# Optimization experiments

Hardware: AMD Instinct MI355X
Metric: run time of the kernel (lower is better)

## Reference

```python
import jax, jax.numpy as jnp
import numpy as np
from jax import lax

L = 4          # num_layers
DIM = 1024
HEADS = 4
DH = DIM // HEADS
MLP_H = 4 * DIM
EPS = 1e-5
SCALE = 1.0 / (DIM ** 0.5)  # note: module scales by 1/sqrt(dim), not 1/sqrt(head_dim)


def layer_norm(x, g, b):
    mu = jnp.mean(x, axis=-1, keepdims=True)
    var = jnp.var(x, axis=-1, keepdims=True)
    return (x - mu) * jax.lax.rsqrt(var + EPS) * g + b


def setup_inputs() -> dict:
    key = jax.random.key(0)
    ks = jax.random.split(key, 12)
    s = 0.02
    img = jax.random.normal(ks[0], (2, 2, 16, 192, 192), dtype=jnp.float32)
    conv_w = jax.random.normal(ks[1], (DIM, 2, 2, 8, 8), dtype=jnp.float32) * s
    conv_b = jnp.zeros((DIM,), jnp.float32)
    n_tokens = 24 * 24 * 8
    pos = jax.random.normal(ks[2], (1, n_tokens, DIM), dtype=jnp.float32) * s
    ln1_g = jnp.ones((L, DIM), jnp.float32); ln1_b = jnp.zeros((L, DIM), jnp.float32)
    ln2_g = jnp.ones((L, DIM), jnp.float32); ln2_b = jnp.zeros((L, DIM), jnp.float32)
    qkv_w = jax.random.normal(ks[3], (L, DIM, 3 * DIM), dtype=jnp.float32) * s
    out_w = jax.random.normal(ks[4], (L, DIM, DIM), dtype=jnp.float32) * s
    out_b = jnp.zeros((L, DIM), jnp.float32)
    fc1_w = jax.random.normal(ks[5], (L, DIM, MLP_H), dtype=jnp.float32) * s
    fc1_b = jnp.zeros((L, MLP_H), jnp.float32)
    fc2_w = jax.random.normal(ks[6], (L, MLP_H, DIM), dtype=jnp.float32) * s
    fc2_b = jnp.zeros((L, DIM), jnp.float32)
    lnf_g = jnp.ones((DIM,), jnp.float32); lnf_b = jnp.zeros((DIM,), jnp.float32)
    return dict(img=img, conv_w=conv_w, conv_b=conv_b, pos=pos,
                ln1_g=ln1_g, ln1_b=ln1_b, qkv_w=qkv_w, out_w=out_w, out_b=out_b,
                ln2_g=ln2_g, ln2_b=ln2_b, fc1_w=fc1_w, fc1_b=fc1_b,
                fc2_w=fc2_w, fc2_b=fc2_b, lnf_g=lnf_g, lnf_b=lnf_b)


def reference(img, conv_w, conv_b, pos, ln1_g, ln1_b, qkv_w, out_w, out_b,
              ln2_g, ln2_b, fc1_w, fc1_b, fc2_w, fc2_b, lnf_g, lnf_b):
    # Patch embed: Conv3d stride==kernel, NCDHW
    p = lax.conv_general_dilated(img, conv_w, window_strides=(2, 8, 8),
                                 padding='VALID',
                                 dimension_numbers=('NCDHW', 'OIDHW', 'NCDHW'))
    p = p + conv_b[None, :, None, None, None]
    b = p.shape[0]
    x = p.reshape(b, DIM, -1).transpose(0, 2, 1)  # (b, n, dim), n = D*H*W order
    x = x + pos

    for i in range(L):
        x1 = layer_norm(x, ln1_g[i], ln1_b[i])
        n = x1.shape[1]
        qkv = (x1 @ qkv_w[i]).reshape(b, n, 3, HEADS, DH)
        q, k, v = (qkv[:, :, j].transpose(0, 2, 1, 3) for j in range(3))  # (b,h,n,dh)
        dot = jnp.einsum('bhnd,bhmd->bhnm', q, k) * SCALE
        attn = jax.nn.softmax(dot, axis=-1)
        o = jnp.einsum('bhnm,bhmd->bhnd', attn, v)
        o = o.transpose(0, 2, 1, 3).reshape(b, n, DIM)
        x = x + (o @ out_w[i] + out_b[i])

        x2 = layer_norm(x, ln2_g[i], ln2_b[i])
        h = jax.nn.gelu(x2 @ fc1_w[i] + fc1_b[i], approximate=False)
        x = x + (h @ fc2_w[i] + fc2_b[i])

    return layer_norm(x, lnf_g, lnf_b)
```

## Files before the change

kernel.cpp:

```cpp
#include <hip/hip_runtime.h>


typedef unsigned short u16;
typedef __bf16 bf16v8 __attribute__((ext_vector_type(8)));
typedef float f32v4 __attribute__((ext_vector_type(4)));
typedef float f32x16 __attribute__((ext_vector_type(16)));

#define NTOK   4608
#define TTOT   9216
#define DIMD   1024
#define H3     3072
#define MLPH   4096
#define NHEAD  4
#define DHEAD  256
#define NLAYER 4
#define KVB    32
#define NKT    (NTOK / KVB)

__device__ __forceinline__ u16 f2bf(float f) {
  unsigned u = __float_as_uint(f);
  u += 0x7fffu + ((u >> 16) & 1u);
  return (u16)(u >> 16);
}
__device__ __forceinline__ float bf2f(u16 b) {
  return __uint_as_float(((unsigned)b) << 16);
}
__device__ __forceinline__ void gload16(const void* g, void* l) {
  __builtin_amdgcn_global_load_lds((__attribute__((address_space(1))) void*)g,
                                   (__attribute__((address_space(3))) void*)l,
                                   16, 0, 0);
}

__global__ __launch_bounds__(256) void transpose_w(
    const float* __restrict__ src, u16* __restrict__ dst, int R, int C) {
  __shared__ float tile[32][33];
  const int c0 = blockIdx.x * 32, r0 = blockIdx.y * 32;
  const int tx = threadIdx.x, ty = threadIdx.y;
#pragma unroll
  for (int i = 0; i < 32; i += 8)
    tile[ty + i][tx] = src[(size_t)(r0 + ty + i) * C + c0 + tx];
  __syncthreads();
#pragma unroll
  for (int i = 0; i < 32; i += 8)
    dst[(size_t)(c0 + ty + i) * R + r0 + tx] = f2bf(tile[tx][ty + i]);
}

__global__ __launch_bounds__(256) void convert_bf16(
    const float* __restrict__ src, u16* __restrict__ dst, int n) {
  int i = blockIdx.x * 256 + threadIdx.x;
  if (i < n) dst[i] = f2bf(src[i]);
}

__global__ __launch_bounds__(256) void patch_extract(
    const float* __restrict__ img, u16* __restrict__ A) {
  const int t = blockIdx.x;
  const int k = threadIdx.x;
  const int b = t / NTOK, r = t % NTOK;
  const int d = r / 576, r2 = r % 576;
  const int hh = r2 / 24, ww = r2 % 24;
  const int ci = k >> 7, k2 = k & 127;
  const int kd = k2 >> 6, k3 = k2 & 63;
  const int kh = k3 >> 3, kw = k3 & 7;
  const size_t idx =
      ((size_t)((b * 2 + ci) * 16 + (2 * d + kd))) * (192 * 192) +
      (size_t)(8 * hh + kh) * 192 + (8 * ww + kw);
  A[(size_t)t * 256 + k] = f2bf(img[idx]);
}

template <int OUTF32>
__global__ __launch_bounds__(256) void ln_kernel(
    const float* __restrict__ x, const float* __restrict__ g,
    const float* __restrict__ bta, void* __restrict__ out) {
  const size_t row = blockIdx.x;
  const int t = threadIdx.x;
  const float4 v = ((const float4*)(x + row * DIMD))[t];
  float s = v.x + v.y + v.z + v.w;
  float ss = v.x * v.x + v.y * v.y + v.z * v.z + v.w * v.w;
#pragma unroll
  for (int o = 32; o; o >>= 1) {
    s += __shfl_xor(s, o, 64);
    ss += __shfl_xor(ss, o, 64);
  }
  __shared__ float sh[8];
  if ((t & 63) == 0) { sh[t >> 6] = s; sh[4 + (t >> 6)] = ss; }
  __syncthreads();
  s = sh[0] + sh[1] + sh[2] + sh[3];
  ss = sh[4] + sh[5] + sh[6] + sh[7];
  const float mu = s * (1.f / DIMD);
  const float rs = rsqrtf(ss * (1.f / DIMD) - mu * mu + 1e-5f);
  const float4 gg = ((const float4*)g)[t];
  const float4 bb = ((const float4*)bta)[t];
  const float y0 = (v.x - mu) * rs * gg.x + bb.x;
  const float y1 = (v.y - mu) * rs * gg.y + bb.y;
  const float y2 = (v.z - mu) * rs * gg.z + bb.z;
  const float y3 = (v.w - mu) * rs * gg.w + bb.w;
  if (OUTF32) {
    float4 o4; o4.x = y0; o4.y = y1; o4.z = y2; o4.w = y3;
    ((float4*)out)[row * 256 + t] = o4;
  } else {
    ushort4 o4;
    o4.x = f2bf(y0); o4.y = f2bf(y1); o4.z = f2bf(y2); o4.w = f2bf(y3);
    ((ushort4*)out)[row * 256 + t] = o4;
  }
}

__global__ __launch_bounds__(256) void transpose_v(
    const u16* __restrict__ qkv, u16* __restrict__ vT) {
  const int bh = blockIdx.z, b = bh >> 2, h = bh & 3;
  const u16* src = qkv + (size_t)b * NTOK * H3 + 2048 + h * DHEAD;
  u16* dst = vT + (size_t)bh * DHEAD * NTOK;
  __shared__ u16 tile[32][33];
  const int t0 = blockIdx.x * 32, d0 = blockIdx.y * 32;
  const int tx = threadIdx.x, ty = threadIdx.y;
#pragma unroll
  for (int i = 0; i < 32; i += 8)
    tile[ty + i][tx] = src[(size_t)(t0 + ty + i) * H3 + d0 + tx];
  __syncthreads();
#pragma unroll
  for (int i = 0; i < 32; i += 8)
    dst[(size_t)(d0 + ty + i) * NTOK + t0 + tx] = tile[tx][ty + i];
}

__global__ __launch_bounds__(512, 2) void flash_attn(
    const u16* __restrict__ qkv, const u16* __restrict__ vT,
    u16* __restrict__ obuf) {
  __shared__ __align__(16) u16 Ks[2][2][KVB * 256];
  __shared__ __align__(16) u16 Vs[2][2][128 * 64];

  const int tid = threadIdx.x;
  const int lane = tid & 63, w = tid >> 6;
  const int c = lane & 31, h32 = lane >> 5;
  const int bh = blockIdx.x & 7, b = bh >> 2, h = bh & 3;
  const int t0 = (blockIdx.x >> 3) * 256;

  const u16* qkv_b = qkv + (size_t)b * NTOK * H3;
  const u16* vt_bh = vT + (size_t)bh * (size_t)DHEAD * NTOK;
  const int kcol = DIMD + h * DHEAD;
  const int rep = (c >> 3) & 1;
  const int csw = (((c & 7) ^ (rep << 2)) << 4);

  bf16v8 qf[16];
  {
    const u16* qrow = qkv_b + (size_t)(t0 + w * 32 + c) * H3 + h * DHEAD + h32 * 8;
#pragma unroll
    for (int ks = 0; ks < 16; ks++)
      qf[ks] = *reinterpret_cast<const bf16v8*>(qrow + ks * 16);
  }

  f32x16 o[8];
#pragma unroll
  for (int dt = 0; dt < 8; dt++)
#pragma unroll
    for (int r = 0; r < 16; r++) o[dt][r] = 0.f;
  float m = -1e30f, l = 0.f;

  auto stage = [&](int kt) {
    const int buf = kt & 1;
    const int kt0 = kt * KVB;
#pragma unroll
    for (int rp = 0; rp < 2; rp++) {
      const int ph = rp << 2;
#pragma unroll
      for (int i = 0; i < 2; i++) {
        const int q = i * 512 + tid;
        const int row = q >> 5;
        const int cb = ((q & 31) * 16) ^ ((((row & 7) ^ ph)) << 4);
        gload16(qkv_b + (size_t)(kt0 + row) * H3 + kcol + (cb >> 1),
                (char*)&Ks[buf][rp][0] + (size_t)q * 16);
      }
#pragma unroll
      for (int i = 0; i < 2; i++) {
        const int q = i * 512 + tid;
        const int rr = q >> 3;
        const int p = ((q & 7) * 16) ^ ((((rr & 7) ^ ph)) << 4);
        const int d = rr + ((p >> 6) << 7);
        gload16(vt_bh + (size_t)d * NTOK + kt0 + ((p & 63) >> 1),
                (char*)&Vs[buf][rp][0] + (size_t)q * 16);
      }
    }
  };

  stage(0);

  for (int kt = 0; kt < NKT; kt++) {
    __syncthreads();
    if (kt + 1 < NKT) stage(kt + 1);

    const char* kb = (const char*)&Ks[kt & 1][rep][0];
    const char* vb = (const char*)&Vs[kt & 1][rep][0];

    f32x16 st;
#pragma unroll
    for (int r = 0; r < 16; r++) st[r] = 0.f;
    const char* krow = kb + c * 512;
    __builtin_amdgcn_s_setprio(1);
#pragma unroll
    for (int ks = 0; ks < 16; ks++) {
      const bf16v8 kf =
          *reinterpret_cast<const bf16v8*>(krow + ((ks * 32 + h32 * 16) ^ csw));
      st = __builtin_amdgcn_mfma_f32_32x32x16_bf16(kf, qf[ks], st, 0, 0, 0);
    }
    __builtin_amdgcn_s_setprio(0);

    float mx = st[0];
#pragma unroll
    for (int r = 1; r < 16; r++) mx = fmaxf(mx, st[r]);
    mx = fmaxf(mx, __shfl_xor(mx, 32, 64));
    const float pm = mx * 0.03125f;
    if (__any(pm > m + 8.f)) {
      const float mn = fmaxf(m, pm);
      const float corr = __expf(m - mn);
      m = mn; l *= corr;
#pragma unroll
      for (int dt = 0; dt < 8; dt++)
#pragma unroll
        for (int r = 0; r < 16; r++) o[dt][r] *= corr;
    }
    float sum = 0.f;
#pragma unroll
    for (int r = 0; r < 16; r++) {
      const float p = __expf(st[r] * 0.03125f - m);
      st[r] = p; sum += p;
    }
    sum += __shfl_xor(sum, 32, 64);
    l += sum;

#pragma unroll
    for (int s = 0; s < 2; s++) {
      const int rb = s * 8;
      float z[4];
#pragma unroll
      for (int k = 0; k < 4; k++) {
        const float y = h32 ? st[rb + k] : st[rb + 4 + k];
        z[k] = __shfl_xor(y, 32, 64);
      }
      union { u16 u[8]; bf16v8 v; } pb;
#pragma unroll
      for (int k = 0; k < 4; k++) {
        pb.u[k]     = f2bf(h32 ? z[k] : st[rb + k]);
        pb.u[4 + k] = f2bf(h32 ? st[rb + 4 + k] : z[k]);
      }
      __builtin_amdgcn_s_setprio(1);
#pragma unroll
      for (int dt = 0; dt < 8; dt++) {
        const int rr = (dt & 3) * 32 + c;
        const int byte = (((dt >> 2) * 64 + s * 32 + h32 * 16)) ^ csw;
        const bf16v8 vf = *reinterpret_cast<const bf16v8*>(vb + rr * 128 + byte);
        o[dt] = __builtin_amdgcn_mfma_f32_32x32x16_bf16(vf, pb.v, o[dt], 0, 0, 0);
      }
      __builtin_amdgcn_s_setprio(0);
    }
  }

  const float rl = 1.f / l;
  u16* orow = obuf + (size_t)(b * NTOK + t0 + w * 32 + c) * DIMD + h * DHEAD;
#pragma unroll
  for (int dt = 0; dt < 8; dt++) {
#pragma unroll
    for (int rq = 0; rq < 4; rq++) {
      ushort4 v4;
      v4.x = f2bf(o[dt][rq * 4 + 0] * rl);
      v4.y = f2bf(o[dt][rq * 4 + 1] * rl);
      v4.z = f2bf(o[dt][rq * 4 + 2] * rl);
      v4.w = f2bf(o[dt][rq * 4 + 3] * rl);
      *reinterpret_cast<ushort4*>(orow + dt * 32 + rq * 8 + h32 * 4) = v4;
    }
  }
}

template <int EPI>
__global__ __launch_bounds__(256) void gemm_bt(
    const u16* __restrict__ A, int lda,
    const u16* __restrict__ Bt, int ldb,
    int K, void* __restrict__ Cp, int ldc,
    const float* __restrict__ bias, const float* __restrict__ extra,
    float scale) {
  __shared__ __align__(16) u16 As[128 * 32];
  __shared__ __align__(16) u16 Bs[128 * 32];
  const int tid = threadIdx.x;
  const int bm = blockIdx.x, bn = blockIdx.y;

  const int c0 = tid, c1 = tid + 256;
  const u16* Ab = A + (size_t)(bm * 128) * lda;
  const u16* Bb = Bt + (size_t)(bn * 128) * ldb;
  const size_t a0 = (size_t)(c0 >> 2) * lda + (c0 & 3) * 8;
  const size_t a1 = (size_t)(c1 >> 2) * lda + (c1 & 3) * 8;
  const size_t b0 = (size_t)(c0 >> 2) * ldb + (c0 & 3) * 8;
  const size_t b1 = (size_t)(c1 >> 2) * ldb + (c1 & 3) * 8;

  const int lane = tid & 63;
  const int wv = tid >> 6;
  const int wm = (wv >> 1) * 64;
  const int wn = (wv & 1) * 64;
  const int fr = lane & 15;
  const int fk = (lane >> 4) * 8;

  f32v4 acc[4][4];
#pragma unroll
  for (int m = 0; m < 4; m++)
#pragma unroll
    for (int n = 0; n < 4; n++) acc[m][n] = (f32v4){0.f, 0.f, 0.f, 0.f};

  for (int k0 = 0; k0 < K; k0 += 32) {
    __syncthreads();
    gload16(Ab + a0 + k0, As + (size_t)c0 * 8);
    gload16(Ab + a1 + k0, As + (size_t)c1 * 8);
    gload16(Bb + b0 + k0, Bs + (size_t)c0 * 8);
    gload16(Bb + b1 + k0, Bs + (size_t)c1 * 8);
    __syncthreads();

    bf16v8 af[4], bq[4];
#pragma unroll
    for (int m = 0; m < 4; m++)
      af[m] = *reinterpret_cast<const bf16v8*>(&As[(wm + m * 16 + fr) * 32 + fk]);
#pragma unroll
    for (int n = 0; n < 4; n++)
      bq[n] = *reinterpret_cast<const bf16v8*>(&Bs[(wn + n * 16 + fr) * 32 + fk]);
#pragma unroll
    for (int m = 0; m < 4; m++)
#pragma unroll
      for (int n = 0; n < 4; n++)
        acc[m][n] =
            __builtin_amdgcn_mfma_f32_16x16x32_bf16(af[m], bq[n], acc[m][n], 0, 0, 0);
  }

  const int rbase = bm * 128 + wm + (lane >> 4) * 4;
  const int cbase = bn * 128 + wn + fr;
#pragma unroll
  for (int m = 0; m < 4; m++) {
#pragma unroll
    for (int n = 0; n < 4; n++) {
      const int col = cbase + n * 16;
#pragma unroll
      for (int j = 0; j < 4; j++) {
        const int rowi = rbase + m * 16 + j;
        const float v = acc[m][n][j];
        if (EPI == 0) {
          ((u16*)Cp)[(size_t)rowi * ldc + col] = f2bf(v);
        } else if (EPI == 2) {
          float* p = (float*)Cp + (size_t)rowi * ldc + col;
          *p += v + bias[col];
        } else if (EPI == 3) {
          float t = v + bias[col];
          t = 0.5f * t * (1.f + erff(t * 0.70710678118654752f));
          ((u16*)Cp)[(size_t)rowi * ldc + col] = f2bf(t);
        } else {
          ((float*)Cp)[(size_t)rowi * ldc + col] =
              v + bias[col] + extra[(size_t)(rowi % NTOK) * DIMD + col];
        }
      }
    }
  }
}

#define SZ_QKVT ((size_t)H3 * DIMD * 2)
#define SZ_OUTT ((size_t)DIMD * DIMD * 2)
#define SZ_FC1T ((size_t)MLPH * DIMD * 2)
#define SZ_FC2T ((size_t)DIMD * MLPH * 2)
#define SZ_CONVW ((size_t)DIMD * 256 * 2)
#define SZ_X ((size_t)TTOT * DIMD * 4)
#define SZ_XO ((size_t)TTOT * DIMD * 2)
#define SZ_BIGA ((size_t)TTOT * H3 * 2 + (size_t)8 * DHEAD * NTOK * 2)

#define OFF_QKVT ((size_t)0)
#define OFF_OUTT (OFF_QKVT + SZ_QKVT)
#define OFF_FC1T (OFF_OUTT + SZ_OUTT)
#define OFF_FC2T (OFF_FC1T + SZ_FC1T)
#define OFF_CONVW (OFF_FC2T + SZ_FC2T)
#define OFF_X (OFF_CONVW + SZ_CONVW)
#define OFF_XO (OFF_X + SZ_X)
#define OFF_BIGA (OFF_XO + SZ_XO)
#define WS_NEED (OFF_BIGA + SZ_BIGA)

extern "C" void kernel_launch(void* const* d_in, const int* in_sizes, int n_in,
                              void* d_out, int out_size, void* d_ws, size_t ws_size,
                              hipStream_t stream) {
  const float* img = (const float*)d_in[0];
  const float* conv_w = (const float*)d_in[1];
  const float* conv_b = (const float*)d_in[2];
  const float* pos = (const float*)d_in[3];
  const float* ln1_g = (const float*)d_in[4];
  const float* ln1_b = (const float*)d_in[5];
  const float* qkv_w = (const float*)d_in[6];
  const float* out_w = (const float*)d_in[7];
  const float* out_b = (const float*)d_in[8];
  const float* ln2_g = (const float*)d_in[9];
  const float* ln2_b = (const float*)d_in[10];
  const float* fc1_w = (const float*)d_in[11];
  const float* fc1_b = (const float*)d_in[12];
  const float* fc2_w = (const float*)d_in[13];
  const float* fc2_b = (const float*)d_in[14];
  const float* lnf_g = (const float*)d_in[15];
  const float* lnf_b = (const float*)d_in[16];
  float* out = (float*)d_out;

  if (ws_size < WS_NEED) return;

  char* ws = (char*)d_ws;
  u16* qkvT = (u16*)(ws + OFF_QKVT);
  u16* outT = (u16*)(ws + OFF_OUTT);
  u16* fc1T = (u16*)(ws + OFF_FC1T);
  u16* fc2T = (u16*)(ws + OFF_FC2T);
  u16* convW = (u16*)(ws + OFF_CONVW);
  float* x = (float*)(ws + OFF_X);
  u16* x1 = (u16*)(ws + OFF_XO);
  u16* obuf = (u16*)(ws + OFF_XO);
  u16* qkv = (u16*)(ws + OFF_BIGA);
  u16* vT = (u16*)(ws + OFF_BIGA + (size_t)TTOT * H3 * 2);
  u16* hbuf = (u16*)(ws + OFF_BIGA);
  u16* patchA = (u16*)(ws + OFF_BIGA);

  const dim3 tb(32, 8);

  convert_bf16<<<1024, 256, 0, stream>>>(conv_w, convW, DIMD * 256);
  patch_extract<<<TTOT, 256, 0, stream>>>(img, patchA);
  gemm_bt<4><<<dim3(TTOT / 128, DIMD / 128, 1), 256, 0, stream>>>(
      patchA, 256, convW, 256, 256, x, DIMD, conv_b, pos, 1.f);

  for (int l = 0; l < NLAYER; l++) {
    transpose_w<<<dim3(H3 / 32, DIMD / 32, 1), tb, 0, stream>>>(
        qkv_w + (size_t)l * DIMD * H3, qkvT, DIMD, H3);
    transpose_w<<<dim3(DIMD / 32, DIMD / 32, 1), tb, 0, stream>>>(
        out_w + (size_t)l * DIMD * DIMD, outT, DIMD, DIMD);
    transpose_w<<<dim3(MLPH / 32, DIMD / 32, 1), tb, 0, stream>>>(
        fc1_w + (size_t)l * DIMD * MLPH, fc1T, DIMD, MLPH);
    transpose_w<<<dim3(DIMD / 32, MLPH / 32, 1), tb, 0, stream>>>(
        fc2_w + (size_t)l * MLPH * DIMD, fc2T, MLPH, DIMD);

    ln_kernel<0><<<TTOT, 256, 0, stream>>>(x, ln1_g + l * DIMD, ln1_b + l * DIMD, x1);
    gemm_bt<0><<<dim3(TTOT / 128, H3 / 128, 1), 256, 0, stream>>>(
        x1, DIMD, qkvT, DIMD, DIMD, qkv, H3, nullptr, nullptr, 1.f);
    transpose_v<<<dim3(NTOK / 32, DHEAD / 32, 8), tb, 0, stream>>>(qkv, vT);

    flash_attn<<<dim3(18 * 8, 1, 1), 512, 0, stream>>>(qkv, vT, obuf);

    gemm_bt<2><<<dim3(TTOT / 128, DIMD / 128, 1), 256, 0, stream>>>(
        obuf, DIMD, outT, DIMD, DIMD, x, DIMD, out_b + l * DIMD, nullptr, 1.f);
    ln_kernel<0><<<TTOT, 256, 0, stream>>>(x, ln2_g + l * DIMD, ln2_b + l * DIMD, x1);
    gemm_bt<3><<<dim3(TTOT / 128, MLPH / 128, 1), 256, 0, stream>>>(
        x1, DIMD, fc1T, DIMD, DIMD, hbuf, MLPH, fc1_b + l * MLPH, nullptr, 1.f);
    gemm_bt<2><<<dim3(TTOT / 128, DIMD / 128, 1), 256, 0, stream>>>(
        hbuf, MLPH, fc2T, MLPH, MLPH, x, DIMD, fc2_b + l * DIMD, nullptr, 1.f);
  }

  ln_kernel<1><<<TTOT, 256, 0, stream>>>(x, lnf_g, lnf_b, out);
}
```

Measured before the change: 3.242 ms.

## Split attention KV range across two blocks and merge partials

Flash attention now processes 128 query rows per 256-thread block and splits the KV sequence into two halves. This raises the grid from 144 to 576 blocks so the GPU's compute units are better filled. Each split writes unnormalized bf16 partial outputs plus its running max and sum. A new merge kernel combines the two halves with log-sum-exp weights. The cost is extra global traffic, an extra launch, and an added bf16 rounding of the partial outputs before the merge.

```diff
diff --git a/kernel.cpp b/kernel.cpp
--- a/kernel.cpp
+++ b/kernel.cpp
@@ -16,6 +16,9 @@
 #define NLAYER 4
 #define KVB    32
 #define NKT    (NTOK / KVB)
+#define NSPL   2
+#define TPS    (NKT / NSPL)
+#define NQT    36
 
 __device__ __forceinline__ u16 f2bf(float f) {
   unsigned u = __float_as_uint(f);
@@ -121,23 +124,24 @@
     dst[(size_t)(d0 + ty + i) * NTOK + t0 + tx] = tile[tx][ty + i];
 }
 
-__global__ __launch_bounds__(512, 2) void flash_attn(
+__global__ __launch_bounds__(256, 2) void flash_attn(
     const u16* __restrict__ qkv, const u16* __restrict__ vT,
-    u16* __restrict__ obuf) {
-  __shared__ __align__(16) u16 Ks[2][2][KVB * 256];
-  __shared__ __align__(16) u16 Vs[2][2][128 * 64];
+    u16* __restrict__ part, float* __restrict__ ml) {
+  __shared__ __align__(16) u16 Ks[2][KVB * 256];
+  __shared__ __align__(16) u16 Vs[2][128 * 64];
 
   const int tid = threadIdx.x;
   const int lane = tid & 63, w = tid >> 6;
   const int c = lane & 31, h32 = lane >> 5;
   const int bh = blockIdx.x & 7, b = bh >> 2, h = bh & 3;
-  const int t0 = (blockIdx.x >> 3) * 256;
+  const int qs = blockIdx.x >> 3;
+  const int qt = qs % NQT, sp = qs / NQT;
+  const int t0 = qt * 128;
 
   const u16* qkv_b = qkv + (size_t)b * NTOK * H3;
   const u16* vt_bh = vT + (size_t)bh * (size_t)DHEAD * NTOK;
   const int kcol = DIMD + h * DHEAD;
-  const int rep = (c >> 3) & 1;
-  const int csw = (((c & 7) ^ (rep << 2)) << 4);
+  const int csw = (c & 7) << 4;
 
   bf16v8 qf[16];
   {
@@ -158,36 +162,33 @@
     const int buf = kt & 1;
     const int kt0 = kt * KVB;
 #pragma unroll
-    for (int rp = 0; rp < 2; rp++) {
-      const int ph = rp << 2;
-#pragma unroll
-      for (int i = 0; i < 2; i++) {
-        const int q = i * 512 + tid;
-        const int row = q >> 5;
-        const int cb = ((q & 31) * 16) ^ ((((row & 7) ^ ph)) << 4);
-        gload16(qkv_b + (size_t)(kt0 + row) * H3 + kcol + (cb >> 1),
-                (char*)&Ks[buf][rp][0] + (size_t)q * 16);
-      }
-#pragma unroll
-      for (int i = 0; i < 2; i++) {
-        const int q = i * 512 + tid;
-        const int rr = q >> 3;
-        const int p = ((q & 7) * 16) ^ ((((rr & 7) ^ ph)) << 4);
-        const int d = rr + ((p >> 6) << 7);
-        gload16(vt_bh + (size_t)d * NTOK + kt0 + ((p & 63) >> 1),
-                (char*)&Vs[buf][rp][0] + (size_t)q * 16);
-      }
+    for (int i = 0; i < 4; i++) {
+      const int q = i * 256 + tid;
+      const int row = q >> 5;
+      const int cb = ((q & 31) * 16) ^ ((row & 7) << 4);
+      gload16(qkv_b + (size_t)(kt0 + row) * H3 + kcol + (cb >> 1),
+              (char*)&Ks[buf][0] + (size_t)q * 16);
+    }
+#pragma unroll
+    for (int i = 0; i < 4; i++) {
+      const int q = i * 256 + tid;
+      const int rr = q >> 3;
+      const int p = ((q & 7) * 16) ^ ((rr & 7) << 4);
+      const int d = rr + ((p >> 6) << 7);
+      gload16(vt_bh + (size_t)d * NTOK + kt0 + ((p & 63) >> 1),
+              (char*)&Vs[buf][0] + (size_t)q * 16);
     }
   };
 
-  stage(0);
-
-  for (int kt = 0; kt < NKT; kt++) {
+  const int kt_beg = sp * TPS, kt_end = kt_beg + TPS;
+  stage(kt_beg);
+
+  for (int kt = kt_beg; kt < kt_end; kt++) {
     __syncthreads();
-    if (kt + 1 < NKT) stage(kt + 1);
-
-    const char* kb = (const char*)&Ks[kt & 1][rep][0];
-    const char* vb = (const char*)&Vs[kt & 1][rep][0];
+    if (kt + 1 < kt_end) stage(kt + 1);
+
+    const char* kb = (const char*)&Ks[kt & 1][0];
+    const char* vb = (const char*)&Vs[kt & 1][0];
 
     f32x16 st;
 #pragma unroll
@@ -252,20 +253,44 @@
     }
   }
 
-  const float rl = 1.f / l;
-  u16* orow = obuf + (size_t)(b * NTOK + t0 + w * 32 + c) * DIMD + h * DHEAD;
+  const int row = t0 + w * 32 + c;
+  u16* prow = part + ((size_t)(sp * 8 + bh) * NTOK + row) * DHEAD;
 #pragma unroll
   for (int dt = 0; dt < 8; dt++) {
 #pragma unroll
     for (int rq = 0; rq < 4; rq++) {
       ushort4 v4;
-      v4.x = f2bf(o[dt][rq * 4 + 0] * rl);
-      v4.y = f2bf(o[dt][rq * 4 + 1] * rl);
-      v4.z = f2bf(o[dt][rq * 4 + 2] * rl);
-      v4.w = f2bf(o[dt][rq * 4 + 3] * rl);
-      *reinterpret_cast<ushort4*>(orow + dt * 32 + rq * 8 + h32 * 4) = v4;
-    }
-  }
+      v4.x = f2bf(o[dt][rq * 4 + 0]);
+      v4.y = f2bf(o[dt][rq * 4 + 1]);
+      v4.z = f2bf(o[dt][rq * 4 + 2]);
+      v4.w = f2bf(o[dt][rq * 4 + 3]);
+      *reinterpret_cast<ushort4*>(prow + dt * 32 + rq * 8 + h32 * 4) = v4;
+    }
+  }
+  if (h32 == 0) {
+    float* mlrow = ml + ((size_t)(sp * 8 + bh) * NTOK + row) * 2;
+    mlrow[0] = m; mlrow[1] = l;
+  }
+}
+
+__global__ __launch_bounds__(256) void merge_attn(
+    const u16* __restrict__ part, const float* __restrict__ ml,
+    u16* __restrict__ obuf) {
+  const int r = blockIdx.x;
+  const int bh = r / NTOK, row = r % NTOK;
+  const int b = bh >> 2, h = bh & 3;
+  const int d = threadIdx.x;
+  const float m0 = ml[((size_t)(0 * 8 + bh) * NTOK + row) * 2];
+  const float l0 = ml[((size_t)(0 * 8 + bh) * NTOK + row) * 2 + 1];
+  const float m1 = ml[((size_t)(1 * 8 + bh) * NTOK + row) * 2];
+  const float l1 = ml[((size_t)(1 * 8 + bh) * NTOK + row) * 2 + 1];
+  const float mm = fmaxf(m0, m1);
+  const float w0 = __expf(m0 - mm), w1 = __expf(m1 - mm);
+  const float inv = 1.f / (l0 * w0 + l1 * w1);
+  const float p0 = bf2f(part[((size_t)(0 * 8 + bh) * NTOK + row) * DHEAD + d]);
+  const float p1 = bf2f(part[((size_t)(1 * 8 + bh) * NTOK + row) * DHEAD + d]);
+  obuf[((size_t)b * NTOK + row) * DIMD + h * DHEAD + d] =
+      f2bf((p0 * w0 + p1 * w1) * inv);
 }
 
 template <int EPI>
@@ -361,6 +386,8 @@
 #define SZ_X ((size_t)TTOT * DIMD * 4)
 #define SZ_XO ((size_t)TTOT * DIMD * 2)
 #define SZ_BIGA ((size_t)TTOT * H3 * 2 + (size_t)8 * DHEAD * NTOK * 2)
+#define SZ_PART ((size_t)NSPL * 8 * NTOK * DHEAD * 2)
+#define SZ_ML ((size_t)NSPL * 8 * NTOK * 2 * 4)
 
 #define OFF_QKVT ((size_t)0)
 #define OFF_OUTT (OFF_QKVT + SZ_QKVT)
@@ -370,7 +397,9 @@
 #define OFF_X (OFF_CONVW + SZ_CONVW)
 #define OFF_XO (OFF_X + SZ_X)
 #define OFF_BIGA (OFF_XO + SZ_XO)
-#define WS_NEED (OFF_BIGA + SZ_BIGA)
+#define OFF_PART (OFF_BIGA + SZ_BIGA)
+#define OFF_ML (OFF_PART + SZ_PART)
+#define WS_NEED (OFF_ML + SZ_ML)
 
 extern "C" void kernel_launch(void* const* d_in, const int* in_sizes, int n_in,
                               void* d_out, int out_size, void* d_ws, size_t ws_size,
@@ -409,6 +438,8 @@
   u16* vT = (u16*)(ws + OFF_BIGA + (size_t)TTOT * H3 * 2);
   u16* hbuf = (u16*)(ws + OFF_BIGA);
   u16* patchA = (u16*)(ws + OFF_BIGA);
+  u16* part = (u16*)(ws + OFF_PART);
+  float* ml = (float*)(ws + OFF_ML);
 
   const dim3 tb(32, 8);
 
@@ -432,7 +463,8 @@
         x1, DIMD, qkvT, DIMD, DIMD, qkv, H3, nullptr, nullptr, 1.f);
     transpose_v<<<dim3(NTOK / 32, DHEAD / 32, 8), tb, 0, stream>>>(qkv, vT);
 
-    flash_attn<<<dim3(18 * 8, 1, 1), 512, 0, stream>>>(qkv, vT, obuf);
+    flash_attn<<<dim3(NSPL * NQT * 8, 1, 1), 256, 0, stream>>>(qkv, vT, part, ml);
+    merge_attn<<<dim3(8 * NTOK, 1, 1), 256, 0, stream>>>(part, ml, obuf);
 
     gemm_bt<2><<<dim3(TTOT / 128, DIMD / 128, 1), 256, 0, stream>>>(
         obuf, DIMD, outT, DIMD, DIMD, x, DIMD, out_b + l * DIMD, nullptr, 1.f);
```

Result: slower. 3.380 ms (+4.3%).

## Double-buffer GEMM LDS tiles and drop duplicated K/V replicas in attention

Applied to the files above, without the earlier changes.

The GEMM kernel now keeps two LDS buffers for A and B. It issues the global-to-LDS loads for the next K-slice before computing on the current one, so there is one barrier per iteration instead of two and load latency can overlap the MFMA work. This doubles the GEMM's shared memory footprint. In flash attention, K and V tiles are no longer staged twice with two different XOR swizzles. Each tile is loaded once with a single swizzle, which halves staging traffic and LDS use but may increase bank conflicts on the fragment reads.

```diff
diff --git a/kernel.cpp b/kernel.cpp
--- a/kernel.cpp
+++ b/kernel.cpp
@@ -124,8 +124,8 @@
 __global__ __launch_bounds__(512, 2) void flash_attn(
     const u16* __restrict__ qkv, const u16* __restrict__ vT,
     u16* __restrict__ obuf) {
-  __shared__ __align__(16) u16 Ks[2][2][KVB * 256];
-  __shared__ __align__(16) u16 Vs[2][2][128 * 64];
+  __shared__ __align__(16) u16 Ks[2][KVB * 256];
+  __shared__ __align__(16) u16 Vs[2][128 * 64];
 
   const int tid = threadIdx.x;
   const int lane = tid & 63, w = tid >> 6;
@@ -136,8 +136,7 @@
   const u16* qkv_b = qkv + (size_t)b * NTOK * H3;
   const u16* vt_bh = vT + (size_t)bh * (size_t)DHEAD * NTOK;
   const int kcol = DIMD + h * DHEAD;
-  const int rep = (c >> 3) & 1;
-  const int csw = (((c & 7) ^ (rep << 2)) << 4);
+  const int csw = (c & 7) << 4;
 
   bf16v8 qf[16];
   {
@@ -158,25 +157,21 @@
     const int buf = kt & 1;
     const int kt0 = kt * KVB;
 #pragma unroll
-    for (int rp = 0; rp < 2; rp++) {
-      const int ph = rp << 2;
-#pragma unroll
-      for (int i = 0; i < 2; i++) {
-        const int q = i * 512 + tid;
-        const int row = q >> 5;
-        const int cb = ((q & 31) * 16) ^ ((((row & 7) ^ ph)) << 4);
-        gload16(qkv_b + (size_t)(kt0 + row) * H3 + kcol + (cb >> 1),
-                (char*)&Ks[buf][rp][0] + (size_t)q * 16);
-      }
-#pragma unroll
-      for (int i = 0; i < 2; i++) {
-        const int q = i * 512 + tid;
-        const int rr = q >> 3;
-        const int p = ((q & 7) * 16) ^ ((((rr & 7) ^ ph)) << 4);
-        const int d = rr + ((p >> 6) << 7);
-        gload16(vt_bh + (size_t)d * NTOK + kt0 + ((p & 63) >> 1),
-                (char*)&Vs[buf][rp][0] + (size_t)q * 16);
-      }
+    for (int i = 0; i < 2; i++) {
+      const int q = i * 512 + tid;
+      const int row = q >> 5;
+      const int cb = ((q & 31) * 16) ^ ((row & 7) << 4);
+      gload16(qkv_b + (size_t)(kt0 + row) * H3 + kcol + (cb >> 1),
+              (char*)&Ks[buf][0] + (size_t)q * 16);
+    }
+#pragma unroll
+    for (int i = 0; i < 2; i++) {
+      const int q = i * 512 + tid;
+      const int rr = q >> 3;
+      const int p = ((q & 7) * 16) ^ ((rr & 7) << 4);
+      const int d = rr + ((p >> 6) << 7);
+      gload16(vt_bh + (size_t)d * NTOK + kt0 + ((p & 63) >> 1),
+              (char*)&Vs[buf][0] + (size_t)q * 16);
     }
   };
 
@@ -186,8 +181,8 @@
     __syncthreads();
     if (kt + 1 < NKT) stage(kt + 1);
 
-    const char* kb = (const char*)&Ks[kt & 1][rep][0];
-    const char* vb = (const char*)&Vs[kt & 1][rep][0];
+    const char* kb = (const char*)&Ks[kt & 1][0];
+    const char* vb = (const char*)&Vs[kt & 1][0];
 
     f32x16 st;
 #pragma unroll
@@ -240,6 +235,7 @@
         pb.u[k]     = f2bf(h32 ? z[k] : st[rb + k]);
         pb.u[4 + k] = f2bf(h32 ? st[rb + 4 + k] : z[k]);
       }
+
       __builtin_amdgcn_s_setprio(1);
 #pragma unroll
       for (int dt = 0; dt < 8; dt++) {
@@ -275,8 +271,8 @@
     int K, void* __restrict__ Cp, int ldc,
     const float* __restrict__ bias, const float* __restrict__ extra,
     float scale) {
-  __shared__ __align__(16) u16 As[128 * 32];
-  __shared__ __align__(16) u16 Bs[128 * 32];
+  __shared__ __align__(16) u16 As[2][128 * 32];
+  __shared__ __align__(16) u16 Bs[2][128 * 32];
   const int tid = threadIdx.x;
   const int bm = blockIdx.x, bn = blockIdx.y;
 
@@ -295,33 +291,42 @@
   const int fr = lane & 15;
   const int fk = (lane >> 4) * 8;
 
+  auto stage = [&](int k0, int buf) {
+    gload16(Ab + a0 + k0, &As[buf][0] + (size_t)c0 * 8);
+    gload16(Ab + a1 + k0, &As[buf][0] + (size_t)c1 * 8);
+    gload16(Bb + b0 + k0, &Bs[buf][0] + (size_t)c0 * 8);
+    gload16(Bb + b1 + k0, &Bs[buf][0] + (size_t)c1 * 8);
+  };
+
   f32v4 acc[4][4];
 #pragma unroll
   for (int m = 0; m < 4; m++)
 #pragma unroll
     for (int n = 0; n < 4; n++) acc[m][n] = (f32v4){0.f, 0.f, 0.f, 0.f};
 
+  stage(0, 0);
+  __syncthreads();
+
+  int buf = 0;
   for (int k0 = 0; k0 < K; k0 += 32) {
-    __syncthreads();
-    gload16(Ab + a0 + k0, As + (size_t)c0 * 8);
-    gload16(Ab + a1 + k0, As + (size_t)c1 * 8);
-    gload16(Bb + b0 + k0, Bs + (size_t)c0 * 8);
-    gload16(Bb + b1 + k0, Bs + (size_t)c1 * 8);
-    __syncthreads();
+    if (k0 + 32 < K) stage(k0 + 32, buf ^ 1);
 
     bf16v8 af[4], bq[4];
 #pragma unroll
     for (int m = 0; m < 4; m++)
-      af[m] = *reinterpret_cast<const bf16v8*>(&As[(wm + m * 16 + fr) * 32 + fk]);
+      af[m] = *reinterpret_cast<const bf16v8*>(&As[buf][(wm + m * 16 + fr) * 32 + fk]);
 #pragma unroll
     for (int n = 0; n < 4; n++)
-      bq[n] = *reinterpret_cast<const bf16v8*>(&Bs[(wn + n * 16 + fr) * 32 + fk]);
+      bq[n] = *reinterpret_cast<const bf16v8*>(&Bs[buf][(wn + n * 16 + fr) * 32 + fk]);
 #pragma unroll
     for (int m = 0; m < 4; m++)
 #pragma unroll
       for (int n = 0; n < 4; n++)
         acc[m][n] =
             __builtin_amdgcn_mfma_f32_16x16x32_bf16(af[m], bq[n], acc[m][n], 0, 0, 0);
+
+    __syncthreads();
+    buf ^= 1;
   }
 
   const int rbase = bm * 128 + wm + (lane >> 4) * 4;
```

New measurement: 2.864 ms, median of 2. -11.7%, faster.
